# Performance work log

Measured on AMD Instinct MI355X. Metric: run time of the kernel, lower is better.

Reference implementation:

```python
import jax, jax.numpy as jnp
import numpy as np

N = 100000      # nodes
E = 800000      # directed edges (avg degree 8)
D_IN, D_HID, D_OUT = 512, 512, 256


def setup_inputs() -> dict:
    key = jax.random.key(0)
    ks = jax.random.split(key, 6)
    x = jax.random.normal(ks[0], (N, D_IN), dtype=jnp.float32)
    edge_index = jax.random.randint(ks[1], (2, E), 0, N, dtype=jnp.int32)
    W1 = jax.random.normal(ks[2], (D_IN, D_HID), dtype=jnp.float32) * (1.0 / np.sqrt(D_IN))
    b1 = jnp.zeros((D_HID,), dtype=jnp.float32)
    W2 = jax.random.normal(ks[3], (D_HID, D_OUT), dtype=jnp.float32) * (1.0 / np.sqrt(D_HID))
    b2 = jnp.zeros((D_OUT,), dtype=jnp.float32)
    return {"x": x, "edge_index": edge_index, "W1": W1, "b1": b1, "W2": W2, "b2": b2}


def gcn_conv(x, W, b, src, dst, n_nodes):
    # h = X W  (dense transform first, as in PyG GCNConv)
    h = x @ W                                              # [N, D_out]
    # symmetric normalization with self-loops already included in src/dst
    deg = jax.ops.segment_sum(jnp.ones(src.shape[0], dtype=h.dtype), dst,
                              num_segments=n_nodes)        # [N]
    dinv = jnp.where(deg > 0, jax.lax.rsqrt(deg), 0.0)
    norm = dinv[src] * dinv[dst]                           # [E+N]
    # gather -> scale -> scatter-add (message passing)
    msgs = h[src] * norm[:, None]                          # [E+N, D_out]
    out = jax.ops.segment_sum(msgs, dst, num_segments=n_nodes)
    return out + b


def reference(x, edge_index, W1, b1, W2, b2):
    n = x.shape[0]
    loops = jnp.arange(n, dtype=edge_index.dtype)          # add self-loops
    src = jnp.concatenate([edge_index[0], loops])
    dst = jnp.concatenate([edge_index[1], loops])
    h = jax.nn.relu(gcn_conv(x, W1, b1, src, dst, n))
    # F.dropout(training=False) is identity in eval mode
    h = gcn_conv(h, W2, b2, src, dst, n)
    return jax.nn.log_softmax(h, axis=1)
```

## Files before the change

kernel.cpp:

```cpp
#include <hip/hip_runtime.h>
#include <hip/hip_bf16.h>

#define NN   100000
#define NE   800000
#define DIN  512
#define DHID 512
#define DOUT 256
#define SCAN_B 1024
#define NSCAN ((NN + SCAN_B - 1) / SCAN_B)

typedef short  s16x8 __attribute__((ext_vector_type(8)));
typedef float  f32x4 __attribute__((ext_vector_type(4)));

__device__ __forceinline__ float bf2f(unsigned short b) {
    union { unsigned u; float f; } c; c.u = ((unsigned)b) << 16; return c.f;
}
__device__ __forceinline__ unsigned short f2bf(float f) {
    union { float f; unsigned u; } c; c.f = f;
    unsigned u = c.u;
    u += 0x7FFFu + ((u >> 16) & 1u);
    return (unsigned short)(u >> 16);
}

__device__ __forceinline__ void gload_lds16(const void* g, void* l) {
    __builtin_amdgcn_global_load_lds(
        (const __attribute__((address_space(1))) void*)g,
        (__attribute__((address_space(3))) void*)l, 16, 0, 0);
}

__global__ void k_zero2(int* a, int* b) {
    int i = blockIdx.x * 256 + threadIdx.x;
    if (i < NN) { a[i] = 0; b[i] = 0; }
}
__global__ void k_hist(const int* __restrict__ dst, int* __restrict__ cnt) {
    int i = blockIdx.x * 256 + threadIdx.x;
    if (i < NE) atomicAdd(&cnt[dst[i]], 1);
}
__global__ void k_dinv(const int* __restrict__ cnt, float* __restrict__ dinv) {
    int i = blockIdx.x * 256 + threadIdx.x;
    if (i < NN) dinv[i] = rsqrtf((float)cnt[i] + 1.0f);
}
__global__ __launch_bounds__(SCAN_B) void k_scan1(
    const int* __restrict__ cnt, int* __restrict__ rowptr, int* __restrict__ bsums)
{
    __shared__ int sh[SCAN_B];
    const int g = blockIdx.x * SCAN_B + threadIdx.x;
    const int v = (g < NN) ? cnt[g] : 0;
    sh[threadIdx.x] = v;
    __syncthreads();
    for (int off = 1; off < SCAN_B; off <<= 1) {
        int t = (threadIdx.x >= off) ? sh[threadIdx.x - off] : 0;
        __syncthreads();
        sh[threadIdx.x] += t;
        __syncthreads();
    }
    if (g < NN) rowptr[g] = sh[threadIdx.x] - v;
    if (threadIdx.x == SCAN_B - 1) bsums[blockIdx.x] = sh[threadIdx.x];
}
__global__ void k_scan2(int* bsums, int* rowptr) {
    if (threadIdx.x == 0 && blockIdx.x == 0) {
        int run = 0;
        for (int i = 0; i < NSCAN; ++i) { int t = bsums[i]; bsums[i] = run; run += t; }
        rowptr[NN] = run;
    }
}
__global__ __launch_bounds__(SCAN_B) void k_scan3(
    int* __restrict__ rowptr, const int* __restrict__ bsums)
{
    const int g = blockIdx.x * SCAN_B + threadIdx.x;
    if (g < NN) rowptr[g] += bsums[blockIdx.x];
}
__global__ void k_fill(const int* __restrict__ src, const int* __restrict__ dst,
                       const int* __restrict__ rowptr, int* __restrict__ cur,
                       int* __restrict__ col)
{
    int i = blockIdx.x * 256 + threadIdx.x;
    if (i < NE) {
        const int d = dst[i];
        const int slot = rowptr[d] + atomicAdd(&cur[d], 1);
        col[slot] = src[i];
    }
}

__global__ __launch_bounds__(256) void k_x2bf(const float* __restrict__ x,
                                              unsigned short* __restrict__ xb)
{
    const size_t i = (size_t)(blockIdx.x * 256 + threadIdx.x) * 8;
    if (i >= (size_t)NN * DIN) return;
    const float4 v0 = *reinterpret_cast<const float4*>(x + i);
    const float4 v1 = *reinterpret_cast<const float4*>(x + i + 4);
    uint4 r;
    r.x = (unsigned)f2bf(v0.x) | ((unsigned)f2bf(v0.y) << 16);
    r.y = (unsigned)f2bf(v0.z) | ((unsigned)f2bf(v0.w) << 16);
    r.z = (unsigned)f2bf(v1.x) | ((unsigned)f2bf(v1.y) << 16);
    r.w = (unsigned)f2bf(v1.z) | ((unsigned)f2bf(v1.w) << 16);
    *reinterpret_cast<uint4*>(xb + i) = r;
}

template<int NCOLS>
__global__ __launch_bounds__(256) void k_wt(const float* __restrict__ W,
                                            unsigned short* __restrict__ Wt)
{
    const int idx = blockIdx.x * 256 + threadIdx.x;
    if (idx >= 512 * NCOLS) return;
    const int k = idx / NCOLS, n = idx % NCOLS;
    Wt[n * 512 + k] = f2bf(W[idx]);
}

template<int NC>
__global__ __launch_bounds__(256) void k_mfma_gemm(
    const unsigned short* __restrict__ A,
    const unsigned short* __restrict__ Wt,
    const float* __restrict__ dinv,
    unsigned short* __restrict__ Hb,
    int M)
{
    constexpr int K = 512;
    __shared__ __align__(16) unsigned short As[128 * 32];
    __shared__ __align__(16) unsigned short Bs[128 * 32];

    const int bm = blockIdx.x * 128;
    const int bn = blockIdx.y * 128;
    const int t    = threadIdx.x;
    const int lane = t & 63;
    const int wid  = t >> 6;
    const int wr = wid >> 1, wc = wid & 1;

    f32x4 acc[4][4];
    #pragma unroll
    for (int i = 0; i < 4; ++i)
        #pragma unroll
        for (int j = 0; j < 4; ++j)
            acc[i][j] = (f32x4){0.f, 0.f, 0.f, 0.f};

    const int r16 = lane & 15;
    const int kc  = lane >> 4;

    for (int k0 = 0; k0 < K; k0 += 32) {
        #pragma unroll
        for (int i = 0; i < 2; ++i) {
            const int c   = i * 256 + t;
            const int row = c >> 2;
            const int cp  = c & 3;
            const int sc  = cp ^ ((row >> 1) & 3);
            const int gr  = (bm + row < M) ? bm + row : M - 1;
            gload_lds16(A  + (size_t)gr * K + k0 + sc * 8,
                        &As[(size_t)(i * 256 + wid * 64) * 8]);
            gload_lds16(Wt + (size_t)(bn + row) * K + k0 + sc * 8,
                        &Bs[(size_t)(i * 256 + wid * 64) * 8]);
        }
        __syncthreads();

        s16x8 af[4], bf[4];
        #pragma unroll
        for (int i = 0; i < 4; ++i) {
            const int ra = wr * 64 + i * 16 + r16;
            af[i] = *reinterpret_cast<const s16x8*>(
                &As[ra * 32 + ((kc ^ ((ra >> 1) & 3)) * 8)]);
            const int rb = wc * 64 + i * 16 + r16;
            bf[i] = *reinterpret_cast<const s16x8*>(
                &Bs[rb * 32 + ((kc ^ ((rb >> 1) & 3)) * 8)]);
        }
        #pragma unroll
        for (int i = 0; i < 4; ++i)
            #pragma unroll
            for (int j = 0; j < 4; ++j)
                acc[i][j] = __builtin_amdgcn_mfma_f32_16x16x32_bf16(
                    af[i], bf[j], acc[i][j], 0, 0, 0);
        __syncthreads();
    }

    #pragma unroll
    for (int i = 0; i < 4; ++i) {
        #pragma unroll
        for (int r = 0; r < 4; ++r) {
            const int m = bm + wr * 64 + i * 16 + (lane >> 4) * 4 + r;
            if (m >= M) continue;
            const float s = dinv[m];
            #pragma unroll
            for (int j = 0; j < 4; ++j) {
                const int n = bn + wc * 64 + j * 16 + (lane & 15);
                Hb[(size_t)m * NC + n] = f2bf(acc[i][j][r] * s);
            }
        }
    }
}

__device__ __forceinline__ void add8(const uint4 u, float* a) {
    a[0] += bf2f((unsigned short)(u.x));  a[1] += bf2f((unsigned short)(u.x >> 16));
    a[2] += bf2f((unsigned short)(u.y));  a[3] += bf2f((unsigned short)(u.y >> 16));
    a[4] += bf2f((unsigned short)(u.z));  a[5] += bf2f((unsigned short)(u.z >> 16));
    a[6] += bf2f((unsigned short)(u.w));  a[7] += bf2f((unsigned short)(u.w >> 16));
}

__global__ __launch_bounds__(256) void k_pull512(
    const int* __restrict__ rowptr, const int* __restrict__ col,
    const float* __restrict__ dinv, const unsigned short* __restrict__ H,
    const float* __restrict__ bias, unsigned short* __restrict__ Out)
{
    const int node = blockIdx.x * 4 + (threadIdx.x >> 6);
    if (node >= NN) return;
    const int lane = threadIdx.x & 63;

    float a[8] = {0.f, 0.f, 0.f, 0.f, 0.f, 0.f, 0.f, 0.f};
    add8(*reinterpret_cast<const uint4*>(H + (size_t)node * DHID + lane * 8), a);

    const int e0 = rowptr[node], e1 = rowptr[node + 1];
    for (int e = e0; e < e1; ++e) {
        const int s = col[e];
        add8(*reinterpret_cast<const uint4*>(H + (size_t)s * DHID + lane * 8), a);
    }

    const float sc = dinv[node];
    unsigned o[4];
    #pragma unroll
    for (int p = 0; p < 4; ++p) {
        float v0 = a[2 * p]     * sc + bias[lane * 8 + 2 * p];
        float v1 = a[2 * p + 1] * sc + bias[lane * 8 + 2 * p + 1];
        v0 = v0 > 0.f ? v0 : 0.f;
        v1 = v1 > 0.f ? v1 : 0.f;
        o[p] = (unsigned)f2bf(v0) | ((unsigned)f2bf(v1) << 16);
    }
    uint4 r = {o[0], o[1], o[2], o[3]};
    *reinterpret_cast<uint4*>(Out + (size_t)node * DHID + lane * 8) = r;
}

__device__ __forceinline__ void add4(const uint2 u, float* a) {
    a[0] += bf2f((unsigned short)(u.x));  a[1] += bf2f((unsigned short)(u.x >> 16));
    a[2] += bf2f((unsigned short)(u.y));  a[3] += bf2f((unsigned short)(u.y >> 16));
}

__global__ __launch_bounds__(256) void k_pull256_lsm(
    const int* __restrict__ rowptr, const int* __restrict__ col,
    const float* __restrict__ dinv, const unsigned short* __restrict__ H,
    const float* __restrict__ b2, float* __restrict__ out)
{
    const int node = blockIdx.x * 4 + (threadIdx.x >> 6);
    if (node >= NN) return;
    const int lane = threadIdx.x & 63;

    float a[4] = {0.f, 0.f, 0.f, 0.f};
    add4(*reinterpret_cast<const uint2*>(H + (size_t)node * DOUT + lane * 4), a);

    const int e0 = rowptr[node], e1 = rowptr[node + 1];
    for (int e = e0; e < e1; ++e) {
        const int s = col[e];
        add4(*reinterpret_cast<const uint2*>(H + (size_t)s * DOUT + lane * 4), a);
    }

    const float sc = dinv[node];
    float v0 = a[0] * sc + b2[lane * 4 + 0];
    float v1 = a[1] * sc + b2[lane * 4 + 1];
    float v2 = a[2] * sc + b2[lane * 4 + 2];
    float v3 = a[3] * sc + b2[lane * 4 + 3];

    float m = fmaxf(fmaxf(v0, v1), fmaxf(v2, v3));
    #pragma unroll
    for (int off = 32; off > 0; off >>= 1) m = fmaxf(m, __shfl_xor(m, off));
    float s = expf(v0 - m) + expf(v1 - m) + expf(v2 - m) + expf(v3 - m);
    #pragma unroll
    for (int off = 32; off > 0; off >>= 1) s += __shfl_xor(s, off);
    const float lse = m + logf(s);

    float4 r = {v0 - lse, v1 - lse, v2 - lse, v3 - lse};
    *reinterpret_cast<float4*>(out + (size_t)node * DOUT + lane * 4) = r;
}

extern "C" void kernel_launch(void* const* d_in, const int* in_sizes, int n_in,
                              void* d_out, int out_size, void* d_ws, size_t ws_size,
                              hipStream_t stream)
{
    const float* x  = (const float*)d_in[0];
    const int*   ei = (const int*)d_in[1];
    const float* W1 = (const float*)d_in[2];
    const float* b1 = (const float*)d_in[3];
    const float* W2 = (const float*)d_in[4];
    const float* b2 = (const float*)d_in[5];
    float* out = (float*)d_out;

    const int* src = ei;
    const int* dst = ei + NE;

    char* ws = (char*)d_ws;
    int*   cnt    = (int*)(ws);
    int*   cur    = (int*)(ws + (size_t)(1 << 19));
    int*   rowptr = (int*)(ws + (size_t)(1 << 20));
    int*   bsums  = (int*)(ws + (size_t)(3 << 19));
    float* dinv   = (float*)(ws + (size_t)(2 << 20));
    int*   col    = (int*)(ws + (size_t)(3 << 20));
    unsigned short* Wt1 = (unsigned short*)(ws + (size_t)(13 << 19));
    unsigned short* Wt2 = (unsigned short*)(ws + (size_t)(7 << 20));
    unsigned short* P   = (unsigned short*)(ws + (size_t)8   * (1 << 20));
    unsigned short* Q   = (unsigned short*)(ws + (size_t)112 * (1 << 20));
    unsigned short* xb = P, * Hr = P;
    unsigned short* H1 = Q, * H2 = Q;

    const int g256n = (NN + 255) / 256;
    const int g256e = (NE + 255) / 256;

    k_zero2<<<g256n, 256, 0, stream>>>(cnt, cur);
    k_hist <<<g256e, 256, 0, stream>>>(dst, cnt);
    k_dinv <<<g256n, 256, 0, stream>>>(cnt, dinv);
    k_scan1<<<NSCAN, SCAN_B, 0, stream>>>(cnt, rowptr, bsums);
    k_scan2<<<1, 64, 0, stream>>>(bsums, rowptr);
    k_scan3<<<NSCAN, SCAN_B, 0, stream>>>(rowptr, bsums);
    k_fill <<<g256e, 256, 0, stream>>>(src, dst, rowptr, cur, col);

    k_x2bf<<<(int)(((size_t)NN * DIN / 8 + 255) / 256), 256, 0, stream>>>(x, xb);
    k_wt<512><<<(512 * 512 + 255) / 256, 256, 0, stream>>>(W1, Wt1);
    k_wt<256><<<(512 * 256 + 255) / 256, 256, 0, stream>>>(W2, Wt2);

    dim3 g1((NN + 127) / 128, DHID / 128);
    k_mfma_gemm<DHID><<<g1, 256, 0, stream>>>(xb, Wt1, dinv, H1, NN);
    k_pull512<<<(NN + 3) / 4, 256, 0, stream>>>(rowptr, col, dinv, H1, b1, Hr);

    dim3 g2((NN + 127) / 128, DOUT / 128);
    k_mfma_gemm<DOUT><<<g2, 256, 0, stream>>>(Hr, Wt2, dinv, H2, NN);
    k_pull256_lsm<<<(NN + 3) / 4, 256, 0, stream>>>(rowptr, col, dinv, H2, b2, out);
}
```

Measured before the change: 544.7 us.

## Remap GEMM blocks per XCD and batch neighbor loads in pull kernels

The GEMM grid is flattened to 1D and block ids are remapped so consecutive output tiles land on the same XCD. Tiles that share A rows and W columns can then reuse the per-XCD L2. The pull aggregation kernels load up to 64 neighbor indices cooperatively in one coalesced read, broadcast them with shuffles, and issue four row gathers per iteration to raise memory-level parallelism. This adds shuffle overhead and extra code for the fallback path when degree exceeds 64.

Result: faster. 509.3 us (-6.5%).

```diff
diff --git a/kernel.cpp b/kernel.cpp
--- a/kernel.cpp
+++ b/kernel.cpp
@@ -115,12 +115,20 @@
     unsigned short* __restrict__ Hb,
     int M)
 {
-    constexpr int K = 512;
+    constexpr int K  = 512;
+    constexpr int GN = NC / 128;
     __shared__ __align__(16) unsigned short As[128 * 32];
     __shared__ __align__(16) unsigned short Bs[128 * 32];
 
-    const int bm = blockIdx.x * 128;
-    const int bn = blockIdx.y * 128;
+    const int GM  = (M + 127) >> 7;
+    const int nwg = GM * GN;
+    const int bid = blockIdx.x;
+    const int q = nwg >> 3, r = nwg & 7;
+    const int xcd = bid & 7, pos = bid >> 3;
+    const int sbid = (xcd < r ? xcd * (q + 1) : r * (q + 1) + (xcd - r) * q) + pos;
+    const int bm = (sbid / GN) * 128;
+    const int bn = (sbid % GN) * 128;
+
     const int t    = threadIdx.x;
     const int lane = t & 63;
     const int wid  = t >> 6;
@@ -173,14 +181,14 @@
     #pragma unroll
     for (int i = 0; i < 4; ++i) {
         #pragma unroll
-        for (int r = 0; r < 4; ++r) {
-            const int m = bm + wr * 64 + i * 16 + (lane >> 4) * 4 + r;
+        for (int r2 = 0; r2 < 4; ++r2) {
+            const int m = bm + wr * 64 + i * 16 + (lane >> 4) * 4 + r2;
             if (m >= M) continue;
             const float s = dinv[m];
             #pragma unroll
             for (int j = 0; j < 4; ++j) {
                 const int n = bn + wc * 64 + j * 16 + (lane & 15);
-                Hb[(size_t)m * NC + n] = f2bf(acc[i][j][r] * s);
+                Hb[(size_t)m * NC + n] = f2bf(acc[i][j][r2] * s);
             }
         }
     }
@@ -202,12 +210,26 @@
     if (node >= NN) return;
     const int lane = threadIdx.x & 63;
 
+    const int e0  = rowptr[node];
+    const int deg = rowptr[node + 1] - e0;
+    const int myc = (lane < deg) ? col[e0 + lane] : 0;
+
     float a[8] = {0.f, 0.f, 0.f, 0.f, 0.f, 0.f, 0.f, 0.f};
     add8(*reinterpret_cast<const uint4*>(H + (size_t)node * DHID + lane * 8), a);
 
-    const int e0 = rowptr[node], e1 = rowptr[node + 1];
-    for (int e = e0; e < e1; ++e) {
-        const int s = col[e];
+    const int dmax = deg < 64 ? deg : 64;
+    int e = 0;
+    for (; e + 4 <= dmax; e += 4) {
+        const int s0 = __shfl(myc, e + 0), s1 = __shfl(myc, e + 1);
+        const int s2 = __shfl(myc, e + 2), s3 = __shfl(myc, e + 3);
+        const uint4 r0 = *reinterpret_cast<const uint4*>(H + (size_t)s0 * DHID + lane * 8);
+        const uint4 r1 = *reinterpret_cast<const uint4*>(H + (size_t)s1 * DHID + lane * 8);
+        const uint4 r2 = *reinterpret_cast<const uint4*>(H + (size_t)s2 * DHID + lane * 8);
+        const uint4 r3 = *reinterpret_cast<const uint4*>(H + (size_t)s3 * DHID + lane * 8);
+        add8(r0, a); add8(r1, a); add8(r2, a); add8(r3, a);
+    }
+    for (; e < deg; ++e) {
+        const int s = (e < 64) ? __shfl(myc, e) : col[e0 + e];
         add8(*reinterpret_cast<const uint4*>(H + (size_t)s * DHID + lane * 8), a);
     }
 
@@ -239,12 +261,26 @@
     if (node >= NN) return;
     const int lane = threadIdx.x & 63;
 
+    const int e0  = rowptr[node];
+    const int deg = rowptr[node + 1] - e0;
+    const int myc = (lane < deg) ? col[e0 + lane] : 0;
+
     float a[4] = {0.f, 0.f, 0.f, 0.f};
     add4(*reinterpret_cast<const uint2*>(H + (size_t)node * DOUT + lane * 4), a);
 
-    const int e0 = rowptr[node], e1 = rowptr[node + 1];
-    for (int e = e0; e < e1; ++e) {
-        const int s = col[e];
+    const int dmax = deg < 64 ? deg : 64;
+    int e = 0;
+    for (; e + 4 <= dmax; e += 4) {
+        const int s0 = __shfl(myc, e + 0), s1 = __shfl(myc, e + 1);
+        const int s2 = __shfl(myc, e + 2), s3 = __shfl(myc, e + 3);
+        const uint2 r0 = *reinterpret_cast<const uint2*>(H + (size_t)s0 * DOUT + lane * 4);
+        const uint2 r1 = *reinterpret_cast<const uint2*>(H + (size_t)s1 * DOUT + lane * 4);
+        const uint2 r2 = *reinterpret_cast<const uint2*>(H + (size_t)s2 * DOUT + lane * 4);
+        const uint2 r3 = *reinterpret_cast<const uint2*>(H + (size_t)s3 * DOUT + lane * 4);
+        add4(r0, a); add4(r1, a); add4(r2, a); add4(r3, a);
+    }
+    for (; e < deg; ++e) {
+        const int s = (e < 64) ? __shfl(myc, e) : col[e0 + e];
         add4(*reinterpret_cast<const uint2*>(H + (size_t)s * DOUT + lane * 4), a);
     }
 
@@ -262,8 +298,8 @@
     for (int off = 32; off > 0; off >>= 1) s += __shfl_xor(s, off);
     const float lse = m + logf(s);
 
-    float4 r = {v0 - lse, v1 - lse, v2 - lse, v3 - lse};
-    *reinterpret_cast<float4*>(out + (size_t)node * DOUT + lane * 4) = r;
+    float4 rr = {v0 - lse, v1 - lse, v2 - lse, v3 - lse};
+    *reinterpret_cast<float4*>(out + (size_t)node * DOUT + lane * 4) = rr;
 }
 
 extern "C" void kernel_launch(void* const* d_in, const int* in_sizes, int n_in,
@@ -310,11 +346,10 @@
     k_wt<512><<<(512 * 512 + 255) / 256, 256, 0, stream>>>(W1, Wt1);
     k_wt<256><<<(512 * 256 + 255) / 256, 256, 0, stream>>>(W2, Wt2);
 
-    dim3 g1((NN + 127) / 128, DHID / 128);
-    k_mfma_gemm<DHID><<<g1, 256, 0, stream>>>(xb, Wt1, dinv, H1, NN);
+    const int GM = (NN + 127) / 128;
+    k_mfma_gemm<DHID><<<GM * (DHID / 128), 256, 0, stream>>>(xb, Wt1, dinv, H1, NN);
     k_pull512<<<(NN + 3) / 4, 256, 0, stream>>>(rowptr, col, dinv, H1, b1, Hr);
 
-    dim3 g2((NN + 127) / 128, DOUT / 128);
-    k_mfma_gemm<DOUT><<<g2, 256, 0, stream>>>(Hr, Wt2, dinv, H2, NN);
+    k_mfma_gemm<DOUT><<<GM * (DOUT / 128), 256, 0, stream>>>(Hr, Wt2, dinv, H2, NN);
     k_pull256_lsm<<<(NN + 3) / 4, 256, 0, stream>>>(rowptr, col, dinv, H2, b2, out);
 }
```

## Fuse fp32-to-bf16 input conversion into first GEMM and remap blocks per XCD

Applied to the files above, without the earlier changes.

Removes the separate x-to-bf16 pass by having the first GEMM load fp32 A tiles straight into LDS (swizzled) and convert them to bf16 in registers with v_cvt_pk_bf16_f32 before the MFMA. This avoids writing and re-reading a bf16 copy of x. Both GEMMs also switch to a 1D grid with an XCD-aware block remapping, so consecutive tiles land on the same XCD for L2 reuse. In exchange, the first GEMM reads twice the A bytes per tile into LDS and does the conversion inside the main loop.

Result: faster. 531.5 us (-2.4%).

```diff
diff --git a/kernel.cpp b/kernel.cpp
--- a/kernel.cpp
+++ b/kernel.cpp
@@ -21,6 +21,11 @@
     u += 0x7FFFu + ((u >> 16) & 1u);
     return (unsigned short)(u >> 16);
 }
+__device__ __forceinline__ unsigned cvtpk_bf16(float lo, float hi) {
+    unsigned r;
+    asm("v_cvt_pk_bf16_f32 %0, %1, %2" : "=v"(r) : "v"(lo), "v"(hi));
+    return r;
+}
 
 __device__ __forceinline__ void gload_lds16(const void* g, void* l) {
     __builtin_amdgcn_global_load_lds(
@@ -82,21 +87,6 @@
     }
 }
 
-__global__ __launch_bounds__(256) void k_x2bf(const float* __restrict__ x,
-                                              unsigned short* __restrict__ xb)
-{
-    const size_t i = (size_t)(blockIdx.x * 256 + threadIdx.x) * 8;
-    if (i >= (size_t)NN * DIN) return;
-    const float4 v0 = *reinterpret_cast<const float4*>(x + i);
-    const float4 v1 = *reinterpret_cast<const float4*>(x + i + 4);
-    uint4 r;
-    r.x = (unsigned)f2bf(v0.x) | ((unsigned)f2bf(v0.y) << 16);
-    r.y = (unsigned)f2bf(v0.z) | ((unsigned)f2bf(v0.w) << 16);
-    r.z = (unsigned)f2bf(v1.x) | ((unsigned)f2bf(v1.y) << 16);
-    r.w = (unsigned)f2bf(v1.z) | ((unsigned)f2bf(v1.w) << 16);
-    *reinterpret_cast<uint4*>(xb + i) = r;
-}
-
 template<int NCOLS>
 __global__ __launch_bounds__(256) void k_wt(const float* __restrict__ W,
                                             unsigned short* __restrict__ Wt)
@@ -105,6 +95,109 @@
     if (idx >= 512 * NCOLS) return;
     const int k = idx / NCOLS, n = idx % NCOLS;
     Wt[n * 512 + k] = f2bf(W[idx]);
+}
+
+__global__ __launch_bounds__(256) void k_gemm1(
+    const float* __restrict__ A,
+    const unsigned short* __restrict__ Wt,
+    const float* __restrict__ dinv,
+    unsigned short* __restrict__ Hb,
+    int M)
+{
+    constexpr int K = 512, NC = 512, GN = NC / 128;
+    __shared__ __align__(16) float          As[128 * 32];
+    __shared__ __align__(16) unsigned short Bs[128 * 32];
+
+    const int GM  = (M + 127) >> 7;
+    const int nwg = GM * GN;
+    const int bid = blockIdx.x;
+    const int q = nwg >> 3, r = nwg & 7;
+    const int xcd = bid & 7, pos = bid >> 3;
+    const int sbid = (xcd < r ? xcd * (q + 1) : r * (q + 1) + (xcd - r) * q) + pos;
+    const int bm = (sbid / GN) * 128;
+    const int bn = (sbid % GN) * 128;
+
+    const int t    = threadIdx.x;
+    const int lane = t & 63;
+    const int wid  = t >> 6;
+    const int wr = wid >> 1, wc = wid & 1;
+
+    f32x4 acc[4][4];
+    #pragma unroll
+    for (int i = 0; i < 4; ++i)
+        #pragma unroll
+        for (int j = 0; j < 4; ++j)
+            acc[i][j] = (f32x4){0.f, 0.f, 0.f, 0.f};
+
+    const int r16 = lane & 15;
+    const int kc  = lane >> 4;
+
+    for (int k0 = 0; k0 < K; k0 += 32) {
+        #pragma unroll
+        for (int i = 0; i < 4; ++i) {
+            const int c   = i * 256 + t;
+            const int row = c >> 3;
+            const int cp  = c & 7;
+            const int sc  = cp ^ (row & 7);
+            const int gr  = (bm + row < M) ? bm + row : M - 1;
+            gload_lds16(A + (size_t)gr * K + k0 + sc * 4,
+                        &As[(size_t)(i * 256 + wid * 64) * 4]);
+        }
+        #pragma unroll
+        for (int i = 0; i < 2; ++i) {
+            const int c   = i * 256 + t;
+            const int row = c >> 2;
+            const int cp  = c & 3;
+            const int sc  = cp ^ ((row >> 1) & 3);
+            gload_lds16(Wt + (size_t)(bn + row) * K + k0 + sc * 8,
+                        &Bs[(size_t)(i * 256 + wid * 64) * 8]);
+        }
+        __syncthreads();
+
+        s16x8 af[4], bf[4];
+        #pragma unroll
+        for (int i = 0; i < 4; ++i) {
+            const int ra  = wr * 64 + i * 16 + r16;
+            const int swz = ra & 7;
+            const f32x4 lo = *reinterpret_cast<const f32x4*>(
+                &As[ra * 32 + (((2 * kc)     ^ swz) * 4)]);
+            const f32x4 hi = *reinterpret_cast<const f32x4*>(
+                &As[ra * 32 + (((2 * kc + 1) ^ swz) * 4)]);
+            uint4 p;
+            p.x = cvtpk_bf16(lo[0], lo[1]);
+            p.y = cvtpk_bf16(lo[2], lo[3]);
+            p.z = cvtpk_bf16(hi[0], hi[1]);
+            p.w = cvtpk_bf16(hi[2], hi[3]);
+            union { uint4 u; s16x8 s; } cv; cv.u = p;
+            af[i] = cv.s;
+
+            const int rb = wc * 64 + i * 16 + r16;
+            bf[i] = *reinterpret_cast<const s16x8*>(
+                &Bs[rb * 32 + ((kc ^ ((rb >> 1) & 3)) * 8)]);
+        }
+        #pragma unroll
+        for (int i = 0; i < 4; ++i)
+            #pragma unroll
+            for (int j = 0; j < 4; ++j)
+                acc[i][j] = __builtin_amdgcn_mfma_f32_16x16x32_bf16(
+                    af[i], bf[j], acc[i][j], 0, 0, 0);
+        __syncthreads();
+    }
+
+    #pragma unroll
+    for (int i = 0; i < 4; ++i) {
+        #pragma unroll
+        for (int r2 = 0; r2 < 4; ++r2) {
+            const int m = bm + wr * 64 + i * 16 + (lane >> 4) * 4 + r2;
+            if (m >= M) continue;
+            const float s = dinv[m];
+            #pragma unroll
+            for (int j = 0; j < 4; ++j) {
+                const int n = bn + wc * 64 + j * 16 + (lane & 15);
+                Hb[(size_t)m * NC + n] = f2bf(acc[i][j][r2] * s);
+            }
+        }
+    }
 }
 
 template<int NC>
@@ -115,12 +208,20 @@
     unsigned short* __restrict__ Hb,
     int M)
 {
-    constexpr int K = 512;
+    constexpr int K  = 512;
+    constexpr int GN = NC / 128;
     __shared__ __align__(16) unsigned short As[128 * 32];
     __shared__ __align__(16) unsigned short Bs[128 * 32];
 
-    const int bm = blockIdx.x * 128;
-    const int bn = blockIdx.y * 128;
+    const int GM  = (M + 127) >> 7;
+    const int nwg = GM * GN;
+    const int bid = blockIdx.x;
+    const int q = nwg >> 3, r = nwg & 7;
+    const int xcd = bid & 7, pos = bid >> 3;
+    const int sbid = (xcd < r ? xcd * (q + 1) : r * (q + 1) + (xcd - r) * q) + pos;
+    const int bm = (sbid / GN) * 128;
+    const int bn = (sbid % GN) * 128;
+
     const int t    = threadIdx.x;
     const int lane = t & 63;
     const int wid  = t >> 6;
@@ -173,14 +274,14 @@
     #pragma unroll
     for (int i = 0; i < 4; ++i) {
         #pragma unroll
-        for (int r = 0; r < 4; ++r) {
-            const int m = bm + wr * 64 + i * 16 + (lane >> 4) * 4 + r;
+        for (int r2 = 0; r2 < 4; ++r2) {
+            const int m = bm + wr * 64 + i * 16 + (lane >> 4) * 4 + r2;
             if (m >= M) continue;
             const float s = dinv[m];
             #pragma unroll
             for (int j = 0; j < 4; ++j) {
                 const int n = bn + wc * 64 + j * 16 + (lane & 15);
-                Hb[(size_t)m * NC + n] = f2bf(acc[i][j][r] * s);
+                Hb[(size_t)m * NC + n] = f2bf(acc[i][j][r2] * s);
             }
         }
     }
@@ -262,8 +363,8 @@
     for (int off = 32; off > 0; off >>= 1) s += __shfl_xor(s, off);
     const float lse = m + logf(s);
 
-    float4 r = {v0 - lse, v1 - lse, v2 - lse, v3 - lse};
-    *reinterpret_cast<float4*>(out + (size_t)node * DOUT + lane * 4) = r;
+    float4 rr = {v0 - lse, v1 - lse, v2 - lse, v3 - lse};
+    *reinterpret_cast<float4*>(out + (size_t)node * DOUT + lane * 4) = rr;
 }
 
 extern "C" void kernel_launch(void* const* d_in, const int* in_sizes, int n_in,
@@ -290,9 +391,8 @@
     int*   col    = (int*)(ws + (size_t)(3 << 20));
     unsigned short* Wt1 = (unsigned short*)(ws + (size_t)(13 << 19));
     unsigned short* Wt2 = (unsigned short*)(ws + (size_t)(7 << 20));
-    unsigned short* P   = (unsigned short*)(ws + (size_t)8   * (1 << 20));
+    unsigned short* Hr  = (unsigned short*)(ws + (size_t)8   * (1 << 20));
     unsigned short* Q   = (unsigned short*)(ws + (size_t)112 * (1 << 20));
-    unsigned short* xb = P, * Hr = P;
     unsigned short* H1 = Q, * H2 = Q;
 
     const int g256n = (NN + 255) / 256;
@@ -306,15 +406,13 @@
     k_scan3<<<NSCAN, SCAN_B, 0, stream>>>(rowptr, bsums);
     k_fill <<<g256e, 256, 0, stream>>>(src, dst, rowptr, cur, col);
 
-    k_x2bf<<<(int)(((size_t)NN * DIN / 8 + 255) / 256), 256, 0, stream>>>(x, xb);
     k_wt<512><<<(512 * 512 + 255) / 256, 256, 0, stream>>>(W1, Wt1);
     k_wt<256><<<(512 * 256 + 255) / 256, 256, 0, stream>>>(W2, Wt2);
 
-    dim3 g1((NN + 127) / 128, DHID / 128);
-    k_mfma_gemm<DHID><<<g1, 256, 0, stream>>>(xb, Wt1, dinv, H1, NN);
+    const int GM = (NN + 127) / 128;
+    k_gemm1<<<GM * (DHID / 128), 256, 0, stream>>>(x, Wt1, dinv, H1, NN);
     k_pull512<<<(NN + 3) / 4, 256, 0, stream>>>(rowptr, col, dinv, H1, b1, Hr);
 
-    dim3 g2((NN + 127) / 128, DOUT / 128);
-    k_mfma_gemm<DOUT><<<g2, 256, 0, stream>>>(Hr, Wt2, dinv, H2, NN);
+    k_mfma_gemm<DOUT><<<GM * (DOUT / 128), 256, 0, stream>>>(Hr, Wt2, dinv, H2, NN);
     k_pull256_lsm<<<(NN + 3) / 4, 256, 0, stream>>>(rowptr, col, dinv, H2, b2, out);
 }
```
